# Optimization experiments

Measured on AMD Instinct MI355X. Metric: run time of the kernel, lower is better.

The kernel has to match this reference:

```python
import jax, jax.numpy as jnp
import numpy as np

NOISE_STD = 0.05
TAU = 0.2


def setup_inputs() -> dict:
    key = jax.random.key(0)
    ks = jax.random.split(key, 10)
    B, T, I, H, R, O = 64, 1024, 64, 512, 8, 64
    return {
        "u": jax.random.normal(ks[0], (B, T, I), jnp.float32),
        "x0": jax.random.normal(ks[1], (B, H), jnp.float32),
        "noise": jax.random.normal(ks[2], (T, B, H), jnp.float32),
        "L": jax.random.normal(ks[3], (H, R), jnp.float32) * 0.06,
        "M": jax.random.normal(ks[4], (H, R), jnp.float32) * 0.06,
        "N": jax.random.normal(ks[5], (H, R), jnp.float32) * 0.06,
        "W_in": jax.random.normal(ks[6], (H, I), jnp.float32) * 0.06,
        "b_in": jax.random.normal(ks[7], (H,), jnp.float32) * 0.02,
        "W_out": jax.random.normal(ks[8], (O, H), jnp.float32) * 0.06,
        "b_out": jax.random.normal(ks[9], (O,), jnp.float32) * 0.02,
    }


def reference(u, x0, noise, L, M, N, W_in, b_in, W_out, b_out):
    # mode='cont', form='rate': r = tanh(x); x <- x + std*noise + tau*(-x + rec + inp)
    H = L.shape[0]
    scale = 1.0 / (H * H)  # cont mode scaling
    u_tb = jnp.swapaxes(u, 0, 1)  # [T,B,I]
    inp = jnp.einsum("tbi,hi->tbh", u_tb, W_in) + b_in  # precomputed input drive [T,B,H]

    def step(x, inputs):
        inp_t, n_t = inputs
        r = jnp.tanh(x)                                   # [B,H]
        rec = ((r @ M) * (r @ N)) @ L.T * scale           # low-rank bilinear term [B,H]
        x_new = x + NOISE_STD * n_t + TAU * (-x + rec + inp_t)
        return x_new, x_new

    x_last, traj = jax.lax.scan(step, x0, (inp, noise))   # traj: [T,B,H]
    traj = jnp.swapaxes(traj, 0, 1)                        # [B,T,H]
    output = jnp.tanh(traj) @ W_out.T + b_out              # [B,T,O]
    return output, x_last, traj
```

## Files before the change

kernel.cpp:

```cpp
#include <hip/hip_runtime.h>

#define B_ 64
#define T_ 1024
#define I_ 64
#define H_ 512
#define R_ 8
#define O_ 64

__device__ __forceinline__ float ftanh(float x) {
    float e = __builtin_amdgcn_exp2f(x * 2.8853900817779268f);
    return 1.0f - 2.0f * __builtin_amdgcn_rcpf(e + 1.0f);
}

template <int CTRL>
__device__ __forceinline__ float dppmov(float x) {
    return __int_as_float(__builtin_amdgcn_update_dpp(
        0, __float_as_int(x), CTRL, 0xF, 0xF, true));
}

__global__ __launch_bounds__(256) void inp_gemm(
    const float* __restrict__ u, const float* __restrict__ W_in,
    const float* __restrict__ b_in, const float* __restrict__ noise,
    float* __restrict__ drive)
{
    __shared__ float4 su4[64 * 16];
    __shared__ float4 sw4[64 * 17];

    const int tid = threadIdx.x;
    const int t0 = blockIdx.x * 64;
    const int h0 = blockIdx.y * 64;
    const int b  = blockIdx.z;

    const float4* usrc = (const float4*)(u + (size_t)(b * T_ + t0) * I_);
    const float4* wsrc = (const float4*)(W_in + (size_t)h0 * I_);

    #pragma unroll
    for (int k = tid; k < 64 * 16; k += 256) {
        su4[k] = usrc[k];
        sw4[(k >> 4) * 17 + (k & 15)] = wsrc[k];
    }
    __syncthreads();

    const int tg = tid >> 4;
    const int hi = tid & 15;

    float acc[4][4];
    #pragma unroll
    for (int a = 0; a < 4; ++a)
        #pragma unroll
        for (int c = 0; c < 4; ++c) acc[a][c] = 0.0f;

    #pragma unroll
    for (int i4 = 0; i4 < 16; ++i4) {
        float4 uv[4], wv[4];
        #pragma unroll
        for (int a = 0; a < 4; ++a) uv[a] = su4[(tg * 4 + a) * 16 + i4];
        #pragma unroll
        for (int c = 0; c < 4; ++c) wv[c] = sw4[(hi + 16 * c) * 17 + i4];
        #pragma unroll
        for (int a = 0; a < 4; ++a)
            #pragma unroll
            for (int c = 0; c < 4; ++c)
                acc[a][c] += uv[a].x * wv[c].x + uv[a].y * wv[c].y +
                             uv[a].z * wv[c].z + uv[a].w * wv[c].w;
    }

    #pragma unroll
    for (int c = 0; c < 4; ++c) {
        const int h = h0 + hi + 16 * c;
        float bi = b_in[h];
        #pragma unroll
        for (int a = 0; a < 4; ++a) {
            const int t = t0 + tg * 4 + a;
            float nz = noise[((size_t)t * B_ + b) * H_ + h];
            drive[(size_t)(b * T_ + t) * H_ + h] =
                0.2f * (acc[a][c] + bi) + 0.05f * nz;
        }
    }
}

template <int NC>
__global__ __launch_bounds__(256) void scan_chunked(
    const float* __restrict__ x0,
    const float* __restrict__ Lm, const float* __restrict__ Mm,
    const float* __restrict__ Nm,
    const float* __restrict__ drive,
    float* __restrict__ traj, float* __restrict__ xlast)
{
    constexpr int C = T_ / NC;
    constexpr int W = 48;

    const int tid  = threadIdx.x;
    const int ckid = blockIdx.x;
    const int b    = blockIdx.y;
    const int h0   = tid * 2;
    const int lane = tid & 63;
    const int lm   = lane & 15;
    const int gl = ((lm & 1) ? 8 : 0) ^ ((lm & 2) ? 4 : 0) ^
                   ((lm & 4) ? 14 : 0) ^ ((lm & 8) ? 1 : 0);

    float w0[16], w1[16];
    #pragma unroll
    for (int k = 0; k < 16; ++k) {
        const int v = k ^ gl;
        const float* src = (v < 8) ? Mm : Nm;
        const int col = v & 7;
        w0[k] = src[h0 * R_ + col];
        w1[k] = src[(h0 + 1) * R_ + col];
    }
    float l0[8], l1[8];
    const float cs = 0.2f / (512.0f * 512.0f);
    #pragma unroll
    for (int j = 0; j < 8; ++j) {
        l0[j] = Lm[h0 * R_ + j] * cs;
        l1[j] = Lm[(h0 + 1) * R_ + j] * cs;
    }

    const int emit0 = ckid * C;
    const int warm  = (ckid == 0) ? 0 : W;
    const int t0s   = emit0 - warm;
    const int tend  = emit0 + C;

    float2 xv;
    if (ckid == 0) xv = *(const float2*)(x0 + (size_t)b * H_ + h0);
    else           xv = make_float2(0.0f, 0.0f);

    const float2* dbase = (const float2*)drive + (size_t)b * (T_ * (H_ / 2)) + tid;
    float2*       tbase = (float2*)traj  + (size_t)b * (T_ * (H_ / 2)) + tid;

    __shared__ __align__(16) float red[8][16];
    if (tid < 128) ((float*)red)[tid] = 0.0f;
    __syncthreads();

    float2 db[4];
    db[0] = dbase[(size_t)(t0s + 0) * 256];
    db[1] = dbase[(size_t)(t0s + 1) * 256];
    db[2] = dbase[(size_t)(t0s + 2) * 256];
    const float2* pf = dbase + (size_t)(t0s + 3) * 256;
    float2*       st = tbase + (size_t)emit0 * 256;
    float2 xstA, xstB;

#define STEP(T0, SA, XST, EMIT)                                             \
    do {                                                                    \
        const int t_ = (T0);                                                \
        constexpr int SR = ((SA) + 6) & 7;       \
        constexpr int SZ = ((SA) + 4) & 7;     \
        constexpr int DP = ((SA) + 3) & 3;    \
        constexpr int DA = (SA) & 3;           \
                    \
        const float4* rp = (const float4*)(&red[SR][0]);                    \
        const float4 f0 = rp[0], f1 = rp[1], f2 = rp[2], f3 = rp[3];        \
        if (t_ + 3 < tend) db[DP] = *pf;                                    \
        pf += 256;                                                          \
               \
        const float r0 = ftanh(xv.x), r1 = ftanh(xv.y);                     \
        float p[16];                                                        \
        _Pragma("unroll")                                                   \
        for (int k = 0; k < 16; ++k) p[k] = r0 * w0[k] + r1 * w1[k];        \
        _Pragma("unroll")                                                   \
        for (int k = 0; k < 8; ++k) p[k] += dppmov<0xB1>(p[k + 8]);         \
        _Pragma("unroll")                                                   \
        for (int k = 0; k < 4; ++k) p[k] += dppmov<0x4E>(p[k + 4]);         \
        _Pragma("unroll")                                                   \
        for (int k = 0; k < 2; ++k) p[k] += dppmov<0x141>(p[k + 2]);        \
        float s_ = p[0] + dppmov<0x128>(p[1]);                              \
        s_ += __shfl_xor(s_, 16, 64);                                       \
        s_ += __shfl_xor(s_, 32, 64);                                       \
        if (lane < 16) {                                                    \
            red[SZ][lane] = 0.0f;           \
            atomicAdd(&red[SA & 7][gl], s_);     \
        }                                                                   \
                         \
        float prod[8] = { f0.x * f2.x, f0.y * f2.y, f0.z * f2.z, f0.w * f2.w,\
                          f1.x * f3.x, f1.y * f3.y, f1.z * f3.z, f1.w * f3.w };\
        float rec0 = 0.0f, rec1 = 0.0f;                                     \
        _Pragma("unroll")                                                   \
        for (int j = 0; j < 8; ++j) { rec0 += l0[j] * prod[j];              \
                                      rec1 += l1[j] * prod[j]; }            \
                                                          \
        const float2 dv = db[DA];                                           \
        xv.x = fmaf(0.8f, xv.x, dv.x + rec0);                               \
        xv.y = fmaf(0.8f, xv.y, dv.y + rec1);                               \
        if (EMIT) { XST = xv; *st = XST; st += 256; }                       \
          \
        if ((SA) & 1)                                                       \
            asm volatile("s_waitcnt lgkmcnt(0)\n\ts_barrier" ::: "memory"); \
    } while (0)

    for (int k = 0; k < warm; k += 8) {
        STEP(t0s + k + 0, 0, xstA, false);
        STEP(t0s + k + 1, 1, xstB, false);
        STEP(t0s + k + 2, 2, xstA, false);
        STEP(t0s + k + 3, 3, xstB, false);
        STEP(t0s + k + 4, 4, xstA, false);
        STEP(t0s + k + 5, 5, xstB, false);
        STEP(t0s + k + 6, 6, xstA, false);
        STEP(t0s + k + 7, 7, xstB, false);
    }
    for (int k = warm; k < warm + C; k += 8) {
        STEP(t0s + k + 0, 0, xstA, true);
        STEP(t0s + k + 1, 1, xstB, true);
        STEP(t0s + k + 2, 2, xstA, true);
        STEP(t0s + k + 3, 3, xstB, true);
        STEP(t0s + k + 4, 4, xstA, true);
        STEP(t0s + k + 5, 5, xstB, true);
        STEP(t0s + k + 6, 6, xstA, true);
        STEP(t0s + k + 7, 7, xstB, true);
    }
#undef STEP

    if (tend == T_)
        *(float2*)(xlast + (size_t)b * H_ + h0) = xv;
}

__global__ __launch_bounds__(256) void out_gemm(
    const float* __restrict__ traj, const float* __restrict__ W_out,
    const float* __restrict__ b_out, float* __restrict__ out)
{
    __shared__ float4 sa4[64 * 17];
    __shared__ float4 sb4[64 * 17];

    const int tid = threadIdx.x;
    const int t0 = blockIdx.x * 64;
    const int b  = blockIdx.y;
    const int tg = tid >> 4, oi = tid & 15;

    const float4* tsrc = (const float4*)(traj + (size_t)(b * T_ + t0) * H_);
    const float4* wsrc = (const float4*)W_out;

    float acc[4][4];
    #pragma unroll
    for (int a = 0; a < 4; ++a)
        #pragma unroll
        for (int c = 0; c < 4; ++c) acc[a][c] = 0.0f;

    float4 pa[4], pb[4];

#define LOADC(HC)                                                            \
    do {                                                                     \
        _Pragma("unroll")                                                    \
        for (int j = 0; j < 4; ++j) {                                        \
            int k = tid + 256 * j;                                           \
            pa[j] = tsrc[(size_t)(k >> 4) * 128 + (HC) * 16 + (k & 15)];     \
            pb[j] = wsrc[(size_t)(k >> 4) * 128 + (HC) * 16 + (k & 15)];     \
        }                                                                    \
    } while (0)

    LOADC(0);

    for (int hc = 0; hc < 8; ++hc) {
        if (hc > 0) __syncthreads();
        #pragma unroll
        for (int j = 0; j < 4; ++j) {
            int k = tid + 256 * j;
            float4 v = pa[j];
            v.x = ftanh(v.x); v.y = ftanh(v.y); v.z = ftanh(v.z); v.w = ftanh(v.w);
            sa4[(k >> 4) * 17 + (k & 15)] = v;
            sb4[(k >> 4) * 17 + (k & 15)] = pb[j];
        }
        __syncthreads();
        if (hc < 7) LOADC(hc + 1);

        #pragma unroll
        for (int i4 = 0; i4 < 16; ++i4) {
            float4 av[4], bv[4];
            #pragma unroll
            for (int a = 0; a < 4; ++a) av[a] = sa4[(tg * 4 + a) * 17 + i4];
            #pragma unroll
            for (int c = 0; c < 4; ++c) bv[c] = sb4[(oi + 16 * c) * 17 + i4];
            #pragma unroll
            for (int a = 0; a < 4; ++a)
                #pragma unroll
                for (int c = 0; c < 4; ++c)
                    acc[a][c] += av[a].x * bv[c].x + av[a].y * bv[c].y +
                                 av[a].z * bv[c].z + av[a].w * bv[c].w;
        }
    }
#undef LOADC

    #pragma unroll
    for (int c = 0; c < 4; ++c) {
        float bo = b_out[oi + 16 * c];
        #pragma unroll
        for (int a = 0; a < 4; ++a)
            out[(size_t)(b * T_ + t0 + tg * 4 + a) * O_ + oi + 16 * c] =
                acc[a][c] + bo;
    }
}

extern "C" void kernel_launch(void* const* d_in, const int* in_sizes, int n_in,
                              void* d_out, int out_size, void* d_ws, size_t ws_size,
                              hipStream_t stream)
{
    const float* u     = (const float*)d_in[0];
    const float* x0    = (const float*)d_in[1];
    const float* noise = (const float*)d_in[2];
    const float* L     = (const float*)d_in[3];
    const float* M     = (const float*)d_in[4];
    const float* N     = (const float*)d_in[5];
    const float* W_in  = (const float*)d_in[6];
    const float* b_in  = (const float*)d_in[7];
    const float* W_out = (const float*)d_in[8];
    const float* b_out = (const float*)d_in[9];

    float* out   = (float*)d_out;
    float* xlast = out + (size_t)B_ * T_ * O_;
    float* traj  = xlast + (size_t)B_ * H_;

    const size_t drive_bytes = (size_t)B_ * T_ * H_ * sizeof(float);

    if (ws_size >= drive_bytes) {
        float* drive = (float*)d_ws;
        inp_gemm<<<dim3(T_ / 64, H_ / 64, B_), 256, 0, stream>>>(
            u, W_in, b_in, noise, drive);
        scan_chunked<16><<<dim3(16, B_), 256, 0, stream>>>(
            x0, L, M, N, drive, traj, xlast);
    } else {
        inp_gemm<<<dim3(T_ / 64, H_ / 64, B_), 256, 0, stream>>>(
            u, W_in, b_in, noise, traj);
        scan_chunked<1><<<dim3(1, B_), 256, 0, stream>>>(
            x0, L, M, N, traj, traj, xlast);
    }

    out_gemm<<<dim3(T_ / 64, B_), 256, 0, stream>>>(traj, W_out, b_out, out);
}
```

Measured before the change: 560.0 us.

## Use split-bf16 MFMA for output projection GEMM

Replaces the scalar FP32 FMA inner loop of the output projection with bf16 MFMA 16x16x32 instructions. Each operand is split into high and low bf16 halves, and three MFMAs (hi*hi, hi*lo, lo*hi) approximate FP32 accuracy. This is meant to cut the ALU cost of the tanh(traj)@W_out GEMM. It adds conversion work, four LDS tiles, and drops the register prefetch of the next chunk, so global loads no longer overlap compute.

```diff
diff --git a/kernel.cpp b/kernel.cpp
--- a/kernel.cpp
+++ b/kernel.cpp
@@ -7,9 +7,17 @@
 #define R_ 8
 #define O_ 64
 
+typedef __attribute__((ext_vector_type(8))) short bf16x8;
+typedef __attribute__((ext_vector_type(4))) float f32x4;
+
 __device__ __forceinline__ float ftanh(float x) {
     float e = __builtin_amdgcn_exp2f(x * 2.8853900817779268f);
     return 1.0f - 2.0f * __builtin_amdgcn_rcpf(e + 1.0f);
+}
+
+__device__ __forceinline__ unsigned int bfr(float a) {
+    unsigned int u = __float_as_uint(a);
+    return (u + 0x7FFFu + ((u >> 16) & 1u)) >> 16;
 }
 
 template <int CTRL>
@@ -217,74 +225,93 @@
     const float* __restrict__ traj, const float* __restrict__ W_out,
     const float* __restrict__ b_out, float* __restrict__ out)
 {
-    __shared__ float4 sa4[64 * 17];
-    __shared__ float4 sb4[64 * 17];
+    __shared__ __align__(16) unsigned short sa_hi[64 * 72];
+    __shared__ __align__(16) unsigned short sa_lo[64 * 72];
+    __shared__ __align__(16) unsigned short sb_hi[64 * 72];
+    __shared__ __align__(16) unsigned short sb_lo[64 * 72];
 
     const int tid = threadIdx.x;
-    const int t0 = blockIdx.x * 64;
-    const int b  = blockIdx.y;
-    const int tg = tid >> 4, oi = tid & 15;
+    const int t0  = blockIdx.x * 64;
+    const int b   = blockIdx.y;
 
     const float4* tsrc = (const float4*)(traj + (size_t)(b * T_ + t0) * H_);
     const float4* wsrc = (const float4*)W_out;
 
-    float acc[4][4];
-    #pragma unroll
-    for (int a = 0; a < 4; ++a)
-        #pragma unroll
-        for (int c = 0; c < 4; ++c) acc[a][c] = 0.0f;
-
-    float4 pa[4], pb[4];
-
-#define LOADC(HC)                                                            \
-    do {                                                                     \
-        _Pragma("unroll")                                                    \
-        for (int j = 0; j < 4; ++j) {                                        \
-            int k = tid + 256 * j;                                           \
-            pa[j] = tsrc[(size_t)(k >> 4) * 128 + (HC) * 16 + (k & 15)];     \
-            pb[j] = wsrc[(size_t)(k >> 4) * 128 + (HC) * 16 + (k & 15)];     \
-        }                                                                    \
-    } while (0)
-
-    LOADC(0);
-
-    for (int hc = 0; hc < 8; ++hc) {
-        if (hc > 0) __syncthreads();
+    const int lane = tid & 63, wv = tid >> 6;
+    const int r  = lane & 15;
+    const int kq = lane >> 4;
+
+    f32x4 acc[4];
+    #pragma unroll
+    for (int ot = 0; ot < 4; ++ot) acc[ot] = (f32x4){0.f, 0.f, 0.f, 0.f};
+
+    for (int kc = 0; kc < 8; ++kc) {
+        if (kc) __syncthreads();
+
         #pragma unroll
         for (int j = 0; j < 4; ++j) {
-            int k = tid + 256 * j;
-            float4 v = pa[j];
-            v.x = ftanh(v.x); v.y = ftanh(v.y); v.z = ftanh(v.z); v.w = ftanh(v.w);
-            sa4[(k >> 4) * 17 + (k & 15)] = v;
-            sb4[(k >> 4) * 17 + (k & 15)] = pb[j];
+            const int idx = tid + 256 * j;
+            const int rw  = idx >> 4;
+            const int c4  = idx & 15;
+            const int ldd = rw * 72 + c4 * 4;
+
+            float4 va = tsrc[(size_t)rw * 128 + kc * 16 + c4];
+            va.x = ftanh(va.x); va.y = ftanh(va.y);
+            va.z = ftanh(va.z); va.w = ftanh(va.w);
+            unsigned int h0 = bfr(va.x), h1 = bfr(va.y),
+                         h2 = bfr(va.z), h3 = bfr(va.w);
+            unsigned int l0 = bfr(va.x - __uint_as_float(h0 << 16));
+            unsigned int l1 = bfr(va.y - __uint_as_float(h1 << 16));
+            unsigned int l2 = bfr(va.z - __uint_as_float(h2 << 16));
+            unsigned int l3 = bfr(va.w - __uint_as_float(h3 << 16));
+            *(uint2*)&sa_hi[ldd] = make_uint2(h0 | (h1 << 16), h2 | (h3 << 16));
+            *(uint2*)&sa_lo[ldd] = make_uint2(l0 | (l1 << 16), l2 | (l3 << 16));
+
+            float4 vb = wsrc[(size_t)rw * 128 + kc * 16 + c4];
+            unsigned int g0 = bfr(vb.x), g1 = bfr(vb.y),
+                         g2 = bfr(vb.z), g3 = bfr(vb.w);
+            unsigned int m0 = bfr(vb.x - __uint_as_float(g0 << 16));
+            unsigned int m1 = bfr(vb.y - __uint_as_float(g1 << 16));
+            unsigned int m2 = bfr(vb.z - __uint_as_float(g2 << 16));
+            unsigned int m3 = bfr(vb.w - __uint_as_float(g3 << 16));
+            *(uint2*)&sb_hi[ldd] = make_uint2(g0 | (g1 << 16), g2 | (g3 << 16));
+            *(uint2*)&sb_lo[ldd] = make_uint2(m0 | (m1 << 16), m2 | (m3 << 16));
         }
         __syncthreads();
-        if (hc < 7) LOADC(hc + 1);
-
-        #pragma unroll
-        for (int i4 = 0; i4 < 16; ++i4) {
-            float4 av[4], bv[4];
-            #pragma unroll
-            for (int a = 0; a < 4; ++a) av[a] = sa4[(tg * 4 + a) * 17 + i4];
-            #pragma unroll
-            for (int c = 0; c < 4; ++c) bv[c] = sb4[(oi + 16 * c) * 17 + i4];
-            #pragma unroll
-            for (int a = 0; a < 4; ++a)
-                #pragma unroll
-                for (int c = 0; c < 4; ++c)
-                    acc[a][c] += av[a].x * bv[c].x + av[a].y * bv[c].y +
-                                 av[a].z * bv[c].z + av[a].w * bv[c].w;
+
+        #pragma unroll
+        for (int kk = 0; kk < 2; ++kk) {
+            const int k0 = kk * 32 + kq * 8;
+            const bf16x8 aH = *(const bf16x8*)&sa_hi[(wv * 16 + r) * 72 + k0];
+            const bf16x8 aL = *(const bf16x8*)&sa_lo[(wv * 16 + r) * 72 + k0];
+            bf16x8 bH[4], bL[4];
+            #pragma unroll
+            for (int ot = 0; ot < 4; ++ot) {
+                bH[ot] = *(const bf16x8*)&sb_hi[(ot * 16 + r) * 72 + k0];
+                bL[ot] = *(const bf16x8*)&sb_lo[(ot * 16 + r) * 72 + k0];
+            }
+            #pragma unroll
+            for (int ot = 0; ot < 4; ++ot)
+                acc[ot] = __builtin_amdgcn_mfma_f32_16x16x32_bf16(
+                    aH, bH[ot], acc[ot], 0, 0, 0);
+            #pragma unroll
+            for (int ot = 0; ot < 4; ++ot)
+                acc[ot] = __builtin_amdgcn_mfma_f32_16x16x32_bf16(
+                    aH, bL[ot], acc[ot], 0, 0, 0);
+            #pragma unroll
+            for (int ot = 0; ot < 4; ++ot)
+                acc[ot] = __builtin_amdgcn_mfma_f32_16x16x32_bf16(
+                    aL, bH[ot], acc[ot], 0, 0, 0);
         }
     }
-#undef LOADC
-
-    #pragma unroll
-    for (int c = 0; c < 4; ++c) {
-        float bo = b_out[oi + 16 * c];
-        #pragma unroll
-        for (int a = 0; a < 4; ++a)
-            out[(size_t)(b * T_ + t0 + tg * 4 + a) * O_ + oi + 16 * c] =
-                acc[a][c] + bo;
+
+    #pragma unroll
+    for (int ot = 0; ot < 4; ++ot) {
+        const float bo = b_out[ot * 16 + r];
+        #pragma unroll
+        for (int i = 0; i < 4; ++i)
+            out[(size_t)(b * T_ + t0 + wv * 16 + kq * 4 + i) * O_ +
+                ot * 16 + r] = acc[ot][i] + bo;
     }
 }
 
```

Result: faster. 470.8 us (-15.9%).
